# Optimization experiments

Hardware: AMD Instinct MI355X
Metric: run time of the kernel (lower is better)

## Reference

```python
import jax, jax.numpy as jnp
import numpy as np

DIM = 1024
HEAD_DIM = 64
H = DIM // HEAD_DIM
HID = int(DIM * 4.0)
EPS = 0.0  # faithful to source bug: LayerNorm(dim, use_bias=False) sets eps=False==0.0


def layer_norm(x, w):
    m = jnp.mean(x, axis=-1, keepdims=True)
    v = jnp.mean((x - m) ** 2, axis=-1, keepdims=True)
    return (x - m) * jax.lax.rsqrt(v + EPS) * w


def mha(q, k, v, mask):
    # q:[B,H,N,d] k,v:[B,H,M,d] mask:[B,N,M] bool
    scale = HEAD_DIM ** -0.5
    attn = jnp.einsum('bhnd,bhmd->bhnm', q, k) * scale
    attn = jnp.where(mask[:, None], attn, -jnp.inf)
    attn = jax.nn.softmax(attn, axis=-1)
    return jnp.einsum('bhnm,bhmd->bhnd', attn, v)


def split_heads(t, n_split):
    # t:[B,L,n_split*H*d] -> [n_split,B,H,L,d]
    B, L, _ = t.shape
    t = t.reshape(B, L, n_split, H, HEAD_DIM)
    return jnp.transpose(t, (2, 0, 3, 1, 4))


def merge_heads(t):
    B, h, L, d = t.shape
    return jnp.transpose(t, (0, 2, 1, 3)).reshape(B, L, h * d)


def setup_inputs() -> dict:
    key = jax.random.key(0)
    ks = jax.random.split(key, 10)
    B, L, M = 4, 1024, 1024
    s = DIM ** -0.5
    return {
        'x': jax.random.normal(ks[0], (B, L, DIM), jnp.float32),
        'context': jax.random.normal(ks[1], (B, M, DIM), jnp.float32),
        'w_qkv': jax.random.normal(ks[2], (3 * DIM, DIM), jnp.float32) * s,
        'w_sa_proj': jax.random.normal(ks[3], (DIM, DIM), jnp.float32) * s,
        'w_q': jax.random.normal(ks[4], (DIM, DIM), jnp.float32) * s,
        'w_kv': jax.random.normal(ks[5], (2 * DIM, DIM), jnp.float32) * s,
        'w_xa_proj': jax.random.normal(ks[6], (DIM, DIM), jnp.float32) * s,
        'w_mlp1': jax.random.normal(ks[7], (HID, DIM), jnp.float32) * s,
        'w_mlp2': jax.random.normal(ks[8], (DIM, HID), jnp.float32) * HID ** -0.5,
        'ln1_w': jnp.ones((DIM,), jnp.float32),
        'lnq_w': jnp.ones((DIM,), jnp.float32),
        'lnc_w': jnp.ones((DIM,), jnp.float32),
        'ln2_w': jnp.ones((DIM,), jnp.float32),
        'sa_mask': jnp.ones((B, L, L), bool),
        'xa_mask': jnp.ones((B, L, M), bool),
    }


def reference(x, context, w_qkv, w_sa_proj, w_q, w_kv, w_xa_proj, w_mlp1, w_mlp2,
              ln1_w, lnq_w, lnc_w, ln2_w, sa_mask, xa_mask):
    # self-attention
    Xn = layer_norm(x, ln1_w)
    q, k, v = split_heads(Xn @ w_qkv.T, 3)
    sa = merge_heads(mha(q, k, v, sa_mask)) @ w_sa_proj.T
    X = x + sa
    # cross-attention
    Yn = layer_norm(X, lnq_w)
    Cn = layer_norm(context, lnc_w)
    qx = split_heads(Yn @ w_q.T, 1)[0]
    kx, vx = split_heads(Cn @ w_kv.T, 2)
    xa = merge_heads(mha(qx, kx, vx, xa_mask)) @ w_xa_proj.T
    Y = X + xa
    # MLP (exact GELU, as torch nn.GELU default)
    Zn = layer_norm(Y, ln2_w)
    h = jax.nn.gelu(Zn @ w_mlp1.T, approximate=False)
    return Y + h @ w_mlp2.T
```

## Files before the change

kernel.cpp:

```cpp
#include <hip/hip_runtime.h>
#include <hip/hip_bf16.h>


typedef unsigned short u16;
typedef unsigned short u16x8 __attribute__((ext_vector_type(8)));
typedef __bf16 bf16x8 __attribute__((ext_vector_type(8)));
typedef float f32x4 __attribute__((ext_vector_type(4)));

__device__ __forceinline__ u16 f2bits(float f) {
  __hip_bfloat16 h = __float2bfloat16(f);
  return __builtin_bit_cast(u16, h);
}
__device__ __forceinline__ float bits2f(u16 b) {
  return __uint_as_float(((unsigned)b) << 16);
}

__device__ __forceinline__ f32x4 mfma16(u16x8 a, u16x8 b, f32x4 c) {
  return __builtin_amdgcn_mfma_f32_16x16x32_bf16(
      __builtin_bit_cast(bf16x8, a), __builtin_bit_cast(bf16x8, b), c, 0, 0, 0);
}

__device__ __forceinline__ void gload_lds16(void* lds, const void* g) {
  __builtin_amdgcn_global_load_lds(
      (__attribute__((address_space(1))) void*)g,
      (__attribute__((address_space(3))) void*)lds, 16, 0, 0);
}

__device__ __forceinline__ int xcd_swizzle(int orig, int nwg) {
  const int q8 = nwg >> 3, r8 = nwg & 7, xcd = orig & 7;
  return (xcd < r8 ? xcd * (q8 + 1) : r8 * (q8 + 1) + (xcd - r8) * q8) + (orig >> 3);
}

__global__ __launch_bounds__(256) void cvt_f2b_kernel(const float* __restrict__ in,
                                                      u16* __restrict__ out) {
  const size_t i = ((size_t)blockIdx.x * 256 + threadIdx.x) * 4;
  const float4 v = *(const float4*)(in + i);
  ushort4 o;
  o.x = f2bits(v.x); o.y = f2bits(v.y); o.z = f2bits(v.z); o.w = f2bits(v.w);
  *(ushort4*)(out + i) = o;
}

__global__ __launch_bounds__(256) void ln_kernel(const float* __restrict__ in,
                                                 const float* __restrict__ w,
                                                 u16* __restrict__ out) {
  const int row = blockIdx.x;
  const int t = threadIdx.x;
  const float4 v = ((const float4*)(in + (size_t)row * 1024))[t];
  float s = v.x + v.y + v.z + v.w;
#pragma unroll
  for (int m = 1; m < 64; m <<= 1) s += __shfl_xor(s, m);
  __shared__ float red1[4], red2[4];
  const int l = t & 63, wv = t >> 6;
  if (l == 0) red1[wv] = s;
  __syncthreads();
  const float mean = (red1[0] + red1[1] + red1[2] + red1[3]) * (1.0f / 1024.0f);
  const float d0 = v.x - mean, d1 = v.y - mean, d2 = v.z - mean, d3 = v.w - mean;
  float q = d0 * d0 + d1 * d1 + d2 * d2 + d3 * d3;
#pragma unroll
  for (int m = 1; m < 64; m <<= 1) q += __shfl_xor(q, m);
  if (l == 0) red2[wv] = q;
  __syncthreads();
  const float rs = rsqrtf((red2[0] + red2[1] + red2[2] + red2[3]) * (1.0f / 1024.0f));
  const float4 wv4 = ((const float4*)w)[t];
  ushort4 o;
  o.x = f2bits(d0 * rs * wv4.x);
  o.y = f2bits(d1 * rs * wv4.y);
  o.z = f2bits(d2 * rs * wv4.z);
  o.w = f2bits(d3 * rs * wv4.w);
  *(ushort4*)(out + (size_t)row * 1024 + t * 4) = o;
}

template <int EPI>
__global__ __launch_bounds__(512) void gemm256(const u16* __restrict__ A,
                                               const u16* __restrict__ B,
                                               const float* __restrict__ res,
                                               void* __restrict__ outp,
                                               int N, int K, int gx) {
  __shared__ u16 sm[2][2][256 * 64];
  const int tid = threadIdx.x;
  const int l = tid & 63, w = tid >> 6;
  const int wr = w >> 2, wc = w & 3;
  const int lrow = l & 15, lg = l >> 4;
  const int wg = xcd_swizzle(blockIdx.x, gridDim.x);
  const int bn = wg % gx, bm = wg / gx;
  const int srow = tid >> 3;
  const int gslot = (tid & 7) ^ (srow & 7);
  const u16* Ag = A + (size_t)(bm * 256 + srow) * K + gslot * 8;
  const u16* Bg = B + (size_t)(bn * 256 + srow) * K + gslot * 8;
  f32x4 acc[8][4] = {};

#define STAGE256(buf, kt)                                                     \
  {                                                                           \
    _Pragma("unroll") for (int qq = 0; qq < 4; ++qq)                          \
        gload_lds16(&sm[buf][0][qq * 4096 + tid * 8], Ag + (size_t)(qq * 64) * K + (kt)); \
    _Pragma("unroll") for (int qq = 0; qq < 4; ++qq)                          \
        gload_lds16(&sm[buf][1][qq * 4096 + tid * 8], Bg + (size_t)(qq * 64) * K + (kt)); \
  }

  STAGE256(0, 0);
  __syncthreads();
  const int NT = K >> 6;
  int cur = 0;
  for (int t = 0; t < NT; ++t) {
    if (t + 1 < NT) STAGE256(cur ^ 1, (t + 1) << 6);
    const u16* As_ = &sm[cur][0][0];
    const u16* Bs_ = &sm[cur][1][0];
    u16x8 b[2][4];
#pragma unroll
    for (int ks = 0; ks < 2; ++ks)
#pragma unroll
      for (int j = 0; j < 4; ++j)
        b[ks][j] = *(const u16x8*)&Bs_[(wc * 64 + j * 16 + lrow) * 64 +
                                       ((ks * 4 + lg) ^ (lrow & 7)) * 8];
#pragma unroll
    for (int i = 0; i < 8; ++i) {
      const int arow = (wr * 128 + i * 16 + lrow) * 64;
      u16x8 a0 = *(const u16x8*)&As_[arow + ((0 + lg) ^ (lrow & 7)) * 8];
      u16x8 a1 = *(const u16x8*)&As_[arow + ((4 + lg) ^ (lrow & 7)) * 8];
      __builtin_amdgcn_s_setprio(1);
#pragma unroll
      for (int j = 0; j < 4; ++j) {
        acc[i][j] = mfma16(a0, b[0][j], acc[i][j]);
        acc[i][j] = mfma16(a1, b[1][j], acc[i][j]);
      }
      __builtin_amdgcn_s_setprio(0);
    }
    __syncthreads();
    cur ^= 1;
  }
#pragma unroll
  for (int i = 0; i < 8; ++i)
#pragma unroll
    for (int j = 0; j < 4; ++j) {
      const int col = bn * 256 + wc * 64 + j * 16 + lrow;
#pragma unroll
      for (int r = 0; r < 4; ++r) {
        const int row = bm * 256 + wr * 128 + i * 16 + lg * 4 + r;
        const size_t idx = (size_t)row * N + col;
        float v = acc[i][j][r];
        if (EPI == 0) {
          ((u16*)outp)[idx] = f2bits(v);
        } else if (EPI == 1) {
          ((float*)outp)[idx] = res[idx] + v;
        } else {
          float g = 0.5f * v * (1.0f + erff(v * 0.70710678118654752f));
          ((u16*)outp)[idx] = f2bits(g);
        }
      }
    }
}

template <int EPI>
__global__ __launch_bounds__(256) void gemm128(const u16* __restrict__ A,
                                               const u16* __restrict__ B,
                                               const float* __restrict__ res,
                                               void* __restrict__ outp,
                                               int N, int K, int gx) {
  __shared__ u16 sm[2][2][128 * 64];
  const int tid = threadIdx.x;
  const int l = tid & 63, w = tid >> 6;
  const int wr = w >> 1, wc = w & 1;
  const int lrow = l & 15, lg = l >> 4;
  const int wg = xcd_swizzle(blockIdx.x, gridDim.x);
  const int bn = wg % gx, bm = wg / gx;
  const int srow = tid >> 3;
  const int gslot = (tid & 7) ^ (srow & 7);
  const u16* Ag = A + (size_t)(bm * 128 + srow) * K + gslot * 8;
  const u16* Bg = B + (size_t)(bn * 128 + srow) * K + gslot * 8;
  f32x4 acc[4][4] = {};

#define STAGE128(buf, kt)                                                     \
  {                                                                           \
    _Pragma("unroll") for (int qq = 0; qq < 4; ++qq)                          \
        gload_lds16(&sm[buf][0][qq * 2048 + tid * 8], Ag + (size_t)(qq * 32) * K + (kt)); \
    _Pragma("unroll") for (int qq = 0; qq < 4; ++qq)                          \
        gload_lds16(&sm[buf][1][qq * 2048 + tid * 8], Bg + (size_t)(qq * 32) * K + (kt)); \
  }

  STAGE128(0, 0);
  __syncthreads();
  const int NT = K >> 6;
  int cur = 0;
  for (int t = 0; t < NT; ++t) {
    if (t + 1 < NT) STAGE128(cur ^ 1, (t + 1) << 6);
    const u16* As_ = &sm[cur][0][0];
    const u16* Bs_ = &sm[cur][1][0];
    u16x8 b[2][4];
#pragma unroll
    for (int ks = 0; ks < 2; ++ks)
#pragma unroll
      for (int j = 0; j < 4; ++j)
        b[ks][j] = *(const u16x8*)&Bs_[(wc * 64 + j * 16 + lrow) * 64 +
                                       ((ks * 4 + lg) ^ (lrow & 7)) * 8];
#pragma unroll
    for (int i = 0; i < 4; ++i) {
      const int arow = (wr * 64 + i * 16 + lrow) * 64;
      u16x8 a0 = *(const u16x8*)&As_[arow + ((0 + lg) ^ (lrow & 7)) * 8];
      u16x8 a1 = *(const u16x8*)&As_[arow + ((4 + lg) ^ (lrow & 7)) * 8];
      __builtin_amdgcn_s_setprio(1);
#pragma unroll
      for (int j = 0; j < 4; ++j) {
        acc[i][j] = mfma16(a0, b[0][j], acc[i][j]);
        acc[i][j] = mfma16(a1, b[1][j], acc[i][j]);
      }
      __builtin_amdgcn_s_setprio(0);
    }
    __syncthreads();
    cur ^= 1;
  }
#pragma unroll
  for (int i = 0; i < 4; ++i)
#pragma unroll
    for (int j = 0; j < 4; ++j) {
      const int col = bn * 128 + wc * 64 + j * 16 + lrow;
#pragma unroll
      for (int r = 0; r < 4; ++r) {
        const int row = bm * 128 + wr * 64 + i * 16 + lg * 4 + r;
        const size_t idx = (size_t)row * N + col;
        float v = acc[i][j][r];
        if (EPI == 0) {
          ((u16*)outp)[idx] = f2bits(v);
        } else if (EPI == 1) {
          ((float*)outp)[idx] = res[idx] + v;
        } else {
          float g = 0.5f * v * (1.0f + erff(v * 0.70710678118654752f));
          ((u16*)outp)[idx] = f2bits(g);
        }
      }
    }
}

__global__ __launch_bounds__(256) void attn_kernel(const u16* __restrict__ qb,
                                                   const u16* __restrict__ kb,
                                                   const u16* __restrict__ vb,
                                                   u16* __restrict__ ob,
                                                   int qs, int kstr, int vs, int os,
                                                   int H_, int M, float scale) {
  __shared__ u16 Ks[64 * 64];
  __shared__ u16 Vt[64 * 72];
  __shared__ u16 Ps[4][16 * 72];
  const int tid = threadIdx.x;
  const int l = tid & 63, w = tid >> 6;
  const int lrow = l & 15, lg = l >> 4;
  const int bh = blockIdx.y, qt = blockIdx.x;
  const int b = bh / H_, h = bh % H_;
  const u16* qp = qb + (size_t)b * 1024 * qs + h * 64;
  const u16* kp = kb + (size_t)b * M * kstr + h * 64;
  const u16* vp = vb + (size_t)b * M * vs + h * 64;
  u16x8 aq[2];
  {
    const u16* qrow = qp + (size_t)(qt * 64 + w * 16 + lrow) * qs;
#pragma unroll
    for (int ksI = 0; ksI < 2; ++ksI) {
      u16x8 tq = *(const u16x8*)(qrow + ksI * 32 + lg * 8);
#pragma unroll
      for (int j = 0; j < 8; ++j) tq[j] = f2bits(bits2f(tq[j]) * scale);
      aq[ksI] = tq;
    }
  }
  f32x4 oacc[4] = {};
  float mrow[4], lsum[4];
#pragma unroll
  for (int r = 0; r < 4; ++r) { mrow[r] = -3.0e38f; lsum[r] = 0.0f; }
  const int srow = tid >> 3;
  const int kslot = ((tid & 7) ^ (srow & 7)) * 8;
  const int scol = (tid & 7) * 8;
  for (int mt = 0; mt < M; mt += 64) {
    gload_lds16(&Ks[tid * 8],        kp + (size_t)(mt + srow) * kstr + kslot);
    gload_lds16(&Ks[2048 + tid * 8], kp + (size_t)(mt + 32 + srow) * kstr + kslot);
#pragma unroll
    for (int ii = 0; ii < 2; ++ii) {
      const int r0 = srow + ii * 32;
      u16x8 tv = *(const u16x8*)(vp + (size_t)(mt + r0) * vs + scol);
#pragma unroll
      for (int j = 0; j < 8; ++j) Vt[(scol + j) * 72 + r0] = tv[j];
    }
    __syncthreads();
    f32x4 sacc[4] = {};
#pragma unroll
    for (int nt = 0; nt < 4; ++nt)
#pragma unroll
      for (int ksI = 0; ksI < 2; ++ksI) {
        u16x8 bk = *(const u16x8*)&Ks[(nt * 16 + lrow) * 64 +
                                      ((ksI * 4 + lg) ^ (lrow & 7)) * 8];
        sacc[nt] = mfma16(aq[ksI], bk, sacc[nt]);
      }
    float alpha[4];
#pragma unroll
    for (int r = 0; r < 4; ++r) {
      float pm = fmaxf(fmaxf(sacc[0][r], sacc[1][r]), fmaxf(sacc[2][r], sacc[3][r]));
      pm = fmaxf(pm, __shfl_xor(pm, 1));
      pm = fmaxf(pm, __shfl_xor(pm, 2));
      pm = fmaxf(pm, __shfl_xor(pm, 4));
      pm = fmaxf(pm, __shfl_xor(pm, 8));
      const float nm = fmaxf(mrow[r], pm);
      alpha[r] = __expf(mrow[r] - nm);
      mrow[r] = nm;
    }
    float rsum[4] = {0.f, 0.f, 0.f, 0.f};
#pragma unroll
    for (int nt = 0; nt < 4; ++nt)
#pragma unroll
      for (int r = 0; r < 4; ++r) {
        const float p = __expf(sacc[nt][r] - mrow[r]);
        sacc[nt][r] = p;
        rsum[r] += p;
      }
#pragma unroll
    for (int r = 0; r < 4; ++r) {
      float rsv = rsum[r];
      rsv += __shfl_xor(rsv, 1); rsv += __shfl_xor(rsv, 2);
      rsv += __shfl_xor(rsv, 4); rsv += __shfl_xor(rsv, 8);
      lsum[r] = lsum[r] * alpha[r] + rsv;
    }
#pragma unroll
    for (int nt = 0; nt < 4; ++nt)
#pragma unroll
      for (int r = 0; r < 4; ++r)
        Ps[w][(lg * 4 + r) * 72 + nt * 16 + lrow] = f2bits(sacc[nt][r]);
#pragma unroll
    for (int nt = 0; nt < 4; ++nt)
#pragma unroll
      for (int r = 0; r < 4; ++r)
        oacc[nt][r] *= alpha[r];
    u16x8 pa[2];
#pragma unroll
    for (int ksI = 0; ksI < 2; ++ksI)
      pa[ksI] = *(const u16x8*)&Ps[w][lrow * 72 + ksI * 32 + lg * 8];
#pragma unroll
    for (int nt = 0; nt < 4; ++nt)
#pragma unroll
      for (int ksI = 0; ksI < 2; ++ksI) {
        u16x8 bv = *(const u16x8*)&Vt[(nt * 16 + lrow) * 72 + ksI * 32 + lg * 8];
        oacc[nt] = mfma16(pa[ksI], bv, oacc[nt]);
      }
    __syncthreads();
  }
#pragma unroll
  for (int nt = 0; nt < 4; ++nt)
#pragma unroll
    for (int r = 0; r < 4; ++r) {
      const int row = qt * 64 + w * 16 + lg * 4 + r;
      const float v = oacc[nt][r] / lsum[r];
      ob[((size_t)b * 1024 + row) * os + h * 64 + nt * 16 + lrow] = f2bits(v);
    }
}

extern "C" void kernel_launch(void* const* d_in, const int* in_sizes, int n_in,
                              void* d_out, int out_size, void* d_ws, size_t ws_size,
                              hipStream_t stream) {
  (void)in_sizes; (void)n_in; (void)out_size; (void)ws_size;
  const float* x    = (const float*)d_in[0];
  const float* ctx  = (const float*)d_in[1];
  const float* wqkv = (const float*)d_in[2];
  const float* wsa  = (const float*)d_in[3];
  const float* wq   = (const float*)d_in[4];
  const float* wkv  = (const float*)d_in[5];
  const float* wxa  = (const float*)d_in[6];
  const float* wm1  = (const float*)d_in[7];
  const float* wm2  = (const float*)d_in[8];
  const float* ln1  = (const float*)d_in[9];
  const float* lnq  = (const float*)d_in[10];
  const float* lnc  = (const float*)d_in[11];
  const float* ln2  = (const float*)d_in[12];
  float* out = (float*)d_out;
  char* ws = (char*)d_ws;
  const size_t MB = 1024 * 1024;
  u16*   wscr  = (u16*)(ws);
  u16*   Xn    = (u16*)(ws + 8 * MB);
  u16*   qkv   = (u16*)(ws + 16 * MB);
  u16*   attnb = (u16*)(ws + 48 * MB);
  float* Xf    = (float*)(ws + 56 * MB);
  u16*   Yn    = Xn;
  u16*   Cn    = (u16*)(ws + 16 * MB);
  u16*   qx    = attnb;
  u16*   kvx   = (u16*)(ws + 24 * MB);
  u16*   xatt  = (u16*)(ws + 40 * MB);
  u16*   Zn    = Xn;
  u16*   h1    = qkv;

  const dim3 blk(256), blk5(512);
  ln_kernel<<<4096, blk, 0, stream>>>(x, ln1, Xn);
  cvt_f2b_kernel<<<3 * 1024, blk, 0, stream>>>(wqkv, wscr);
  gemm256<0><<<192, blk5, 0, stream>>>(Xn, wscr, nullptr, qkv, 3072, 1024, 12);
  attn_kernel<<<dim3(16, 64), blk, 0, stream>>>(qkv, qkv + 1024, qkv + 2048, attnb,
                                                3072, 3072, 3072, 1024, 16, 1024, 0.125f);
  cvt_f2b_kernel<<<1024, blk, 0, stream>>>(wsa, wscr);
  gemm128<1><<<256, blk, 0, stream>>>(attnb, wscr, x, Xf, 1024, 1024, 8);
  ln_kernel<<<4096, blk, 0, stream>>>(Xf, lnq, Yn);
  ln_kernel<<<4096, blk, 0, stream>>>(ctx, lnc, Cn);
  cvt_f2b_kernel<<<1024, blk, 0, stream>>>(wq, wscr);
  gemm128<0><<<256, blk, 0, stream>>>(Yn, wscr, nullptr, qx, 1024, 1024, 8);
  cvt_f2b_kernel<<<2 * 1024, blk, 0, stream>>>(wkv, wscr);
  gemm256<0><<<128, blk5, 0, stream>>>(Cn, wscr, nullptr, kvx, 2048, 1024, 8);
  attn_kernel<<<dim3(16, 64), blk, 0, stream>>>(qx, kvx, kvx + 1024, xatt,
                                                1024, 2048, 2048, 1024, 16, 1024, 0.125f);
  cvt_f2b_kernel<<<1024, blk, 0, stream>>>(wxa, wscr);
  gemm128<1><<<256, blk, 0, stream>>>(xatt, wscr, Xf, out, 1024, 1024, 8);
  ln_kernel<<<4096, blk, 0, stream>>>(out, ln2, Zn);
  cvt_f2b_kernel<<<4 * 1024, blk, 0, stream>>>(wm1, wscr);
  gemm256<2><<<256, blk5, 0, stream>>>(Zn, wscr, nullptr, h1, 4096, 1024, 16);
  cvt_f2b_kernel<<<4 * 1024, blk, 0, stream>>>(wm2, wscr);
  gemm128<1><<<256, blk, 0, stream>>>(h1, wscr, out, out, 1024, 4096, 8);
}
```

Measured before the change: 576.2 us.

## Transpose QK MFMA so each lane owns one query row, swizzle V tile

The attention kernel swaps the MFMA operands for S so that each lane holds scores for a single query row. This cuts the row max/sum reductions from four per-row 4-step shuffles to one 2-step shuffle per lane. P is now written to LDS as packed 64-bit stores, and the per-row alpha and l values are broadcast with shuffles for the output rescale. The transposed V tile drops its padding in favour of an XOR swizzle to avoid bank conflicts at lower LDS size. The risk is added index arithmetic and shuffle broadcasts, plus swizzle correctness.

After: 501.2 us. -13.0%, faster.

```diff
diff --git a/kernel.cpp b/kernel.cpp
--- a/kernel.cpp
+++ b/kernel.cpp
@@ -237,7 +237,7 @@
                                                    int qs, int kstr, int vs, int os,
                                                    int H_, int M, float scale) {
   __shared__ u16 Ks[64 * 64];
-  __shared__ u16 Vt[64 * 72];
+  __shared__ u16 Vt[64 * 64];
   __shared__ u16 Ps[4][16 * 72];
   const int tid = threadIdx.x;
   const int l = tid & 63, w = tid >> 6;
@@ -251,17 +251,15 @@
   {
     const u16* qrow = qp + (size_t)(qt * 64 + w * 16 + lrow) * qs;
 #pragma unroll
-    for (int ksI = 0; ksI < 2; ++ksI) {
-      u16x8 tq = *(const u16x8*)(qrow + ksI * 32 + lg * 8);
+    for (int ks = 0; ks < 2; ++ks) {
+      u16x8 tq = *(const u16x8*)(qrow + ks * 32 + lg * 8);
 #pragma unroll
       for (int j = 0; j < 8; ++j) tq[j] = f2bits(bits2f(tq[j]) * scale);
-      aq[ksI] = tq;
+      aq[ks] = tq;
     }
   }
   f32x4 oacc[4] = {};
-  float mrow[4], lsum[4];
-#pragma unroll
-  for (int r = 0; r < 4; ++r) { mrow[r] = -3.0e38f; lsum[r] = 0.0f; }
+  float mst = -3.0e38f, lst = 0.0f;
   const int srow = tid >> 3;
   const int kslot = ((tid & 7) ^ (srow & 7)) * 8;
   const int scol = (tid & 7) * 8;
@@ -273,75 +271,81 @@
       const int r0 = srow + ii * 32;
       u16x8 tv = *(const u16x8*)(vp + (size_t)(mt + r0) * vs + scol);
 #pragma unroll
-      for (int j = 0; j < 8; ++j) Vt[(scol + j) * 72 + r0] = tv[j];
+      for (int j = 0; j < 8; ++j) {
+        const int d = scol + j;
+        Vt[d * 64 + (((r0 >> 3) ^ ((tid & 7) + j)) & 7) * 8 + (r0 & 7)] = tv[j];
+      }
     }
     __syncthreads();
     f32x4 sacc[4] = {};
 #pragma unroll
+    for (int km = 0; km < 4; ++km)
+#pragma unroll
+      for (int ks = 0; ks < 2; ++ks) {
+        u16x8 bk = *(const u16x8*)&Ks[(km * 16 + lrow) * 64 +
+                                      ((ks * 4 + lg) ^ (lrow & 7)) * 8];
+        sacc[km] = mfma16(bk, aq[ks], sacc[km]);
+      }
+    float pm = fmaxf(fmaxf(fmaxf(sacc[0][0], sacc[0][1]), fmaxf(sacc[0][2], sacc[0][3])),
+                     fmaxf(fmaxf(sacc[1][0], sacc[1][1]), fmaxf(sacc[1][2], sacc[1][3])));
+    pm = fmaxf(pm, fmaxf(fmaxf(fmaxf(sacc[2][0], sacc[2][1]), fmaxf(sacc[2][2], sacc[2][3])),
+                         fmaxf(fmaxf(sacc[3][0], sacc[3][1]), fmaxf(sacc[3][2], sacc[3][3]))));
+    pm = fmaxf(pm, __shfl_xor(pm, 16));
+    pm = fmaxf(pm, __shfl_xor(pm, 32));
+    const float nm = fmaxf(mst, pm);
+    const float alpha = __expf(mst - nm);
+    mst = nm;
+    float rs = 0.0f;
+#pragma unroll
+    for (int km = 0; km < 4; ++km)
+#pragma unroll
+      for (int r = 0; r < 4; ++r) {
+        const float p = __expf(sacc[km][r] - nm);
+        sacc[km][r] = p;
+        rs += p;
+      }
+    rs += __shfl_xor(rs, 16);
+    rs += __shfl_xor(rs, 32);
+    lst = lst * alpha + rs;
+#pragma unroll
+    for (int km = 0; km < 4; ++km) {
+      uint2 pk2;
+      pk2.x = (unsigned)f2bits(sacc[km][0]) | ((unsigned)f2bits(sacc[km][1]) << 16);
+      pk2.y = (unsigned)f2bits(sacc[km][2]) | ((unsigned)f2bits(sacc[km][3]) << 16);
+      *(uint2*)&Ps[w][lrow * 72 + km * 16 + lg * 4] = pk2;
+    }
+    float af[4];
+#pragma unroll
+    for (int r = 0; r < 4; ++r) af[r] = __shfl(alpha, (l & 48) | ((l >> 4) * 4 + r));
+#pragma unroll
     for (int nt = 0; nt < 4; ++nt)
 #pragma unroll
-      for (int ksI = 0; ksI < 2; ++ksI) {
-        u16x8 bk = *(const u16x8*)&Ks[(nt * 16 + lrow) * 64 +
-                                      ((ksI * 4 + lg) ^ (lrow & 7)) * 8];
-        sacc[nt] = mfma16(aq[ksI], bk, sacc[nt]);
-      }
-    float alpha[4];
-#pragma unroll
-    for (int r = 0; r < 4; ++r) {
-      float pm = fmaxf(fmaxf(sacc[0][r], sacc[1][r]), fmaxf(sacc[2][r], sacc[3][r]));
-      pm = fmaxf(pm, __shfl_xor(pm, 1));
-      pm = fmaxf(pm, __shfl_xor(pm, 2));
-      pm = fmaxf(pm, __shfl_xor(pm, 4));
-      pm = fmaxf(pm, __shfl_xor(pm, 8));
-      const float nm = fmaxf(mrow[r], pm);
-      alpha[r] = __expf(mrow[r] - nm);
-      mrow[r] = nm;
-    }
-    float rsum[4] = {0.f, 0.f, 0.f, 0.f};
-#pragma unroll
-    for (int nt = 0; nt < 4; ++nt)
-#pragma unroll
-      for (int r = 0; r < 4; ++r) {
-        const float p = __expf(sacc[nt][r] - mrow[r]);
-        sacc[nt][r] = p;
-        rsum[r] += p;
-      }
-#pragma unroll
-    for (int r = 0; r < 4; ++r) {
-      float rsv = rsum[r];
-      rsv += __shfl_xor(rsv, 1); rsv += __shfl_xor(rsv, 2);
-      rsv += __shfl_xor(rsv, 4); rsv += __shfl_xor(rsv, 8);
-      lsum[r] = lsum[r] * alpha[r] + rsv;
-    }
-#pragma unroll
-    for (int nt = 0; nt < 4; ++nt)
-#pragma unroll
-      for (int r = 0; r < 4; ++r)
-        Ps[w][(lg * 4 + r) * 72 + nt * 16 + lrow] = f2bits(sacc[nt][r]);
-#pragma unroll
-    for (int nt = 0; nt < 4; ++nt)
-#pragma unroll
-      for (int r = 0; r < 4; ++r)
-        oacc[nt][r] *= alpha[r];
+      for (int r = 0; r < 4; ++r) oacc[nt][r] *= af[r];
     u16x8 pa[2];
 #pragma unroll
-    for (int ksI = 0; ksI < 2; ++ksI)
-      pa[ksI] = *(const u16x8*)&Ps[w][lrow * 72 + ksI * 32 + lg * 8];
-#pragma unroll
-    for (int nt = 0; nt < 4; ++nt)
-#pragma unroll
-      for (int ksI = 0; ksI < 2; ++ksI) {
-        u16x8 bv = *(const u16x8*)&Vt[(nt * 16 + lrow) * 72 + ksI * 32 + lg * 8];
-        oacc[nt] = mfma16(pa[ksI], bv, oacc[nt]);
-      }
+    for (int ks = 0; ks < 2; ++ks)
+      pa[ks] = *(const u16x8*)&Ps[w][lrow * 72 + ks * 32 + lg * 8];
+#pragma unroll
+    for (int nt = 0; nt < 4; ++nt) {
+      const int d = nt * 16 + lrow;
+      const int sig = ((nt * 2 + (lrow >> 3)) + (lrow & 7)) & 7;
+#pragma unroll
+      for (int ks = 0; ks < 2; ++ks) {
+        u16x8 bv = *(const u16x8*)&Vt[d * 64 + (((ks * 4 + lg) ^ sig) & 7) * 8];
+        oacc[nt] = mfma16(pa[ks], bv, oacc[nt]);
+      }
+    }
     __syncthreads();
   }
+  float lf[4];
+#pragma unroll
+  for (int r = 0; r < 4; ++r) lf[r] = __shfl(lst, (l & 48) | ((l >> 4) * 4 + r));
 #pragma unroll
   for (int nt = 0; nt < 4; ++nt)
 #pragma unroll
     for (int r = 0; r < 4; ++r) {
       const int row = qt * 64 + w * 16 + lg * 4 + r;
-      const float v = oacc[nt][r] / lsum[r];
+      const float v = oacc[nt][r] / lf[r];
       ob[((size_t)b * 1024 + row) * os + h * 64 + nt * 16 + lrow] = f2bits(v);
     }
 }
```
